# Kernel tuning notes

Hardware: AMD Instinct MI355X
Metric: run time of the kernel (lower is better)

Reference implementation:

```python
import jax, jax.numpy as jnp
import numpy as np

E = 1024  # embedding_dim
A = 1024  # attention_dim


def setup_inputs() -> dict:
    key = jax.random.key(0)
    k0, k1, k2, k3 = jax.random.split(key, 4)
    embedded = jax.random.normal(k0, (4, 4096, E), dtype=jnp.float32)
    # torch Linear weight is [out, in]; stored here as [in, out] for x @ W
    scale = 1.0 / np.sqrt(E)
    Wk = jax.random.uniform(k1, (E, A), dtype=jnp.float32, minval=-scale, maxval=scale)
    Wq = jax.random.uniform(k2, (E, A), dtype=jnp.float32, minval=-scale, maxval=scale)
    Wv = jax.random.uniform(k3, (E, A), dtype=jnp.float32, minval=-scale, maxval=scale)
    return {"embedded": embedded, "Wk": Wk, "Wq": Wq, "Wv": Wv}


def reference(embedded, Wk, Wq, Wv):
    B, T, C = embedded.shape
    K = embedded @ Wk  # [B,T,A]
    Q = embedded @ Wq
    V = embedded @ Wv
    d_k = Q.shape[-1]
    scores = jnp.einsum('bqa,bka->bqk', Q, K) / jnp.sqrt(jnp.float32(d_k))
    causal = jnp.tril(jnp.ones((T, T), dtype=bool))
    scores = jnp.where(causal, scores, -jnp.inf)
    attn = jax.nn.softmax(scores, axis=-1)
    out = jnp.einsum('bqk,bka->bqa', attn, V)
    return jnp.round(out, decimals=4)
```

## Files before the change

### kernel.cpp

```cpp
#include <hip/hip_runtime.h>
#include <hip/hip_fp16.h>

#define T_SEQ 4096
#define NBATCH 4
#define EDIM 1024
#define ADIM 1024
#define MTOT (NBATCH * T_SEQ)

typedef _Float16 f16x8 __attribute__((ext_vector_type(8)));
typedef float f32x4 __attribute__((ext_vector_type(4)));

#define STAGE(SRC, LD, LDSARR)                                               \
  {                                                                          \
    _Pragma("unroll") for (int t = 0; t < 2; ++t) {                          \
      const int rb = w * 2 + t;                                              \
      const _Float16* gsrc =                                                 \
          (SRC) + (size_t)(rb * 16 + (lane & 15)) * (LD) + (lane >> 4) * 8;  \
      __builtin_amdgcn_global_load_lds(                                      \
          (const __attribute__((address_space(1))) void*)gsrc,               \
          (__attribute__((address_space(3))) void*)&LDSARR[rb * 512], 16,    \
          0, 0);                                                             \
    }                                                                        \
  }

#define FRAG(LDSARR, B4, G) (*(const f16x8*)&LDSARR[((B4) * 4 + (G)) * 128 + lr * 8])

__global__ __launch_bounds__(256) void cast_x(const float* __restrict__ X,
                                              _Float16* __restrict__ Xh) {
  const size_t i = ((size_t)blockIdx.x * 256 + threadIdx.x) * 8;
  float4 a = ((const float4*)(X + i))[0];
  float4 b = ((const float4*)(X + i))[1];
  f16x8 o = {(_Float16)a.x, (_Float16)a.y, (_Float16)a.z, (_Float16)a.w,
             (_Float16)b.x, (_Float16)b.y, (_Float16)b.z, (_Float16)b.w};
  *(f16x8*)(Xh + i) = o;
}

__global__ __launch_bounds__(256) void cast_transpose_w(
    const float* __restrict__ Wk, const float* __restrict__ Wq,
    const float* __restrict__ Wv, _Float16* __restrict__ Wt) {
  __shared__ float tile[32][33];
  const int z = blockIdx.z;
  const float* W = (z == 0) ? Wk : (z == 1) ? Wq : Wv;
  const int n0 = blockIdx.x * 32, k0 = blockIdx.y * 32;
  const int tx = threadIdx.x, ty = threadIdx.y;
#pragma unroll
  for (int yy = 0; yy < 32; yy += 8)
    tile[ty + yy][tx] = W[(size_t)(k0 + ty + yy) * ADIM + n0 + tx];
  __syncthreads();
  _Float16* out = Wt + (size_t)z * EDIM * ADIM;
#pragma unroll
  for (int yy = 0; yy < 32; yy += 8)
    out[(size_t)(n0 + ty + yy) * EDIM + k0 + tx] = (_Float16)tile[tx][ty + yy];
}

__global__ __launch_bounds__(256) void gemm_qkv(
    const _Float16* __restrict__ Xh, const _Float16* __restrict__ Wt,
    _Float16* __restrict__ Qb, _Float16* __restrict__ Kb,
    _Float16* __restrict__ Vt) {
  const int z = blockIdx.z;
  const _Float16* Bt = Wt + (size_t)z * EDIM * ADIM;
  __shared__ __align__(16) _Float16 Al[4096];
  __shared__ __align__(16) _Float16 Bl[4096];
  const int tid = threadIdx.x;
  const int lane = tid & 63, w = tid >> 6;
  const int wm = w >> 1, wn = w & 1;
  const int lr = lane & 15, g = lane >> 4;
  const int h = blockIdx.y * gridDim.x + blockIdx.x;
  const int orig = (h & 7) * 128 + (h >> 3);
  const int m0 = (orig >> 3) * 128, n0 = (orig & 7) * 128;

  f32x4 acc[4][4] = {};

  for (int k0 = 0; k0 < EDIM; k0 += 32) {
    STAGE(Xh + (size_t)m0 * EDIM + k0, EDIM, Al);
    STAGE(Bt + (size_t)n0 * EDIM + k0, EDIM, Bl);
    __syncthreads();
    f16x8 af[4], bf[4];
#pragma unroll
    for (int i = 0; i < 4; i++) af[i] = FRAG(Al, wm * 4 + i, g);
#pragma unroll
    for (int j = 0; j < 4; j++) bf[j] = FRAG(Bl, wn * 4 + j, g);
#pragma unroll
    for (int i = 0; i < 4; i++)
#pragma unroll
      for (int j = 0; j < 4; j++)
        acc[i][j] = __builtin_amdgcn_mfma_f32_16x16x32_f16(af[i], bf[j], acc[i][j], 0, 0, 0);
    __syncthreads();
  }

#pragma unroll
  for (int i = 0; i < 4; i++)
#pragma unroll
    for (int j = 0; j < 4; j++)
#pragma unroll
      for (int r = 0; r < 4; r++) {
        const int row = m0 + wm * 64 + i * 16 + 4 * g + r;
        const int col = n0 + wn * 64 + j * 16 + lr;
        const _Float16 hv = (_Float16)acc[i][j][r];
        if (z == 0)
          Kb[(size_t)row * ADIM + col] = hv;
        else if (z == 1)
          Qb[(size_t)row * ADIM + col] = hv;
        else {
          const int b = row >> 12, tt = row & 4095;
          Vt[((size_t)b * ADIM + col) * T_SEQ + tt] = hv;
        }
      }
}

__global__ __launch_bounds__(256) void gemm_sqk(
    const _Float16* __restrict__ Qb, const _Float16* __restrict__ Kb,
    _Float16* __restrict__ Sb) {
  __shared__ __align__(16) _Float16 Al[4096];
  __shared__ __align__(16) _Float16 Bl[4096];
  const int b = blockIdx.y;
  const int tid = threadIdx.x;
  const int lane = tid & 63, w = tid >> 6;
  const int wm = w >> 1, wn = w & 1;
  const int lr = lane & 15, g = lane >> 4;
  const int h = blockIdx.x;
  const int orig = (h & 7) * 66 + (h >> 3);
  int bi = (int)((sqrtf(8.f * orig + 1.f) - 1.f) * 0.5f);
  while ((bi + 1) * (bi + 2) / 2 <= orig) ++bi;
  while (bi * (bi + 1) / 2 > orig) --bi;
  const int bj = orig - bi * (bi + 1) / 2;
  const int m0 = bi * 128, n0 = bj * 128;
  const _Float16* A = Qb + (size_t)b * T_SEQ * ADIM;
  const _Float16* B = Kb + (size_t)b * T_SEQ * ADIM;

  f32x4 acc[4][4] = {};

  for (int k0 = 0; k0 < ADIM; k0 += 32) {
    STAGE(A + (size_t)m0 * ADIM + k0, ADIM, Al);
    STAGE(B + (size_t)n0 * ADIM + k0, ADIM, Bl);
    __syncthreads();
    f16x8 af[4], bf[4];
#pragma unroll
    for (int i = 0; i < 4; i++) af[i] = FRAG(Al, wm * 4 + i, g);
#pragma unroll
    for (int j = 0; j < 4; j++) bf[j] = FRAG(Bl, wn * 4 + j, g);
#pragma unroll
    for (int i = 0; i < 4; i++)
#pragma unroll
      for (int j = 0; j < 4; j++)
        acc[i][j] = __builtin_amdgcn_mfma_f32_16x16x32_f16(af[i], bf[j], acc[i][j], 0, 0, 0);
    __syncthreads();
  }

  _Float16* Srow = Sb + (size_t)b * T_SEQ * T_SEQ;
#pragma unroll
  for (int i = 0; i < 4; i++)
#pragma unroll
    for (int j = 0; j < 4; j++)
#pragma unroll
      for (int r = 0; r < 4; r++) {
        const int row = m0 + wm * 64 + i * 16 + 4 * g + r;
        const int col = n0 + wn * 64 + j * 16 + lr;
        Srow[(size_t)row * T_SEQ + col] = (_Float16)acc[i][j][r];
      }
}

__global__ __launch_bounds__(512) void softmax_rows(_Float16* __restrict__ S) {
  const int i = blockIdx.x, b = blockIdx.y;
  const int padded = ((i >> 7) + 1) << 7;
  const int tid = threadIdx.x;
  const int lane = tid & 63, w = tid >> 6;
  const int j0 = tid * 8;
  const bool active = j0 < padded;
  _Float16* row = S + ((size_t)b * T_SEQ + i) * T_SEQ;
  const float sm_scale = 0.03125f;

  float v[8];
  float m = -1e30f;
  if (active) {
    f16x8 x = *(const f16x8*)(row + j0);
#pragma unroll
    for (int jj = 0; jj < 8; jj++) {
      const float sv = (j0 + jj <= i) ? (float)x[jj] * sm_scale : -1e30f;
      v[jj] = sv;
      m = fmaxf(m, sv);
    }
  } else {
#pragma unroll
    for (int jj = 0; jj < 8; jj++) v[jj] = -1e30f;
  }
#pragma unroll
  for (int off = 1; off < 64; off <<= 1) m = fmaxf(m, __shfl_xor(m, off));
  __shared__ float redm[8], reds[8];
  if (lane == 0) redm[w] = m;
  __syncthreads();
#pragma unroll
  for (int ww = 0; ww < 8; ww++) m = fmaxf(m, redm[ww]);

  float s = 0.f;
#pragma unroll
  for (int jj = 0; jj < 8; jj++) {
    v[jj] = __expf(v[jj] - m);
    s += v[jj];
  }
#pragma unroll
  for (int off = 1; off < 64; off <<= 1) s += __shfl_xor(s, off);
  if (lane == 0) reds[w] = s;
  __syncthreads();
  s = 0.f;
#pragma unroll
  for (int ww = 0; ww < 8; ww++) s += reds[ww];
  const float inv = 1.f / s;

  if (active) {
    f16x8 o;
#pragma unroll
    for (int jj = 0; jj < 8; jj++) o[jj] = (_Float16)(v[jj] * inv);
    *(f16x8*)(row + j0) = o;
  }
}

__global__ __launch_bounds__(256) void gemm_pv(
    const _Float16* __restrict__ Pb, const _Float16* __restrict__ Vt,
    float* __restrict__ Part, float* __restrict__ Out) {
  __shared__ __align__(16) _Float16 Al[4096];
  __shared__ __align__(16) _Float16 Bl[4096];
  const int b = blockIdx.y;
  const int tid = threadIdx.x;
  const int lane = tid & 63, w = tid >> 6;
  const int wm = w >> 1, wn = w & 1;
  const int lr = lane & 15, g = lane >> 4;
  const int h = blockIdx.x;
  const int orig = (h & 7) * 48 + (h >> 3);
  int by, c, bx;
  if (orig < 128) {
    by = orig >> 3; c = 0; bx = orig & 7;
  } else {
    const int idx = orig - 128;
    by = 16 + (idx >> 4); c = (idx >> 3) & 1; bx = idx & 7;
  }
  const int m0 = by * 128, n0 = bx * 128;
  const int kbeg = c * 2048;
  const int kmax = (by + 1) * 128;
  const int kend = (c == 0) ? (kmax < 2048 ? kmax : 2048) : kmax;
  const _Float16* A = Pb + (size_t)b * T_SEQ * T_SEQ;
  const _Float16* B = Vt + (size_t)b * ADIM * T_SEQ;

  f32x4 acc[4][4] = {};

  for (int k0 = kbeg; k0 < kend; k0 += 32) {
    STAGE(A + (size_t)m0 * T_SEQ + k0, T_SEQ, Al);
    STAGE(B + (size_t)n0 * T_SEQ + k0, T_SEQ, Bl);
    __syncthreads();
    f16x8 af[4], bf[4];
#pragma unroll
    for (int i = 0; i < 4; i++) af[i] = FRAG(Al, wm * 4 + i, g);
#pragma unroll
    for (int j = 0; j < 4; j++) bf[j] = FRAG(Bl, wn * 4 + j, g);
#pragma unroll
    for (int i = 0; i < 4; i++)
#pragma unroll
      for (int j = 0; j < 4; j++)
        acc[i][j] = __builtin_amdgcn_mfma_f32_16x16x32_f16(af[i], bf[j], acc[i][j], 0, 0, 0);
    __syncthreads();
  }

#pragma unroll
  for (int i = 0; i < 4; i++)
#pragma unroll
    for (int j = 0; j < 4; j++)
#pragma unroll
      for (int r = 0; r < 4; r++) {
        const int row = m0 + wm * 64 + i * 16 + 4 * g + r;
        const int col = n0 + wn * 64 + j * 16 + lr;
        if (c == 0)
          Out[((size_t)b * T_SEQ + row) * ADIM + col] = acc[i][j][r];
        else
          Part[((size_t)b * 2048 + (row - 2048)) * ADIM + col] = acc[i][j][r];
      }
}

__global__ __launch_bounds__(256) void reduce_pv(const float* __restrict__ Part,
                                                 float* __restrict__ Out) {
  const size_t id = (size_t)blockIdx.x * 256 + threadIdx.x;
  const int b = (int)(id >> 19);
  const size_t rem = id & 524287;
  const size_t row2 = rem >> 8, coli = rem & 255;
  float4* o = (float4*)Out + ((size_t)(b * 4096 + 2048) + row2) * 256 + coli;
  const float4* p = (const float4*)Part + ((size_t)b * 2048 + row2) * 256 + coli;
  float4 ov = *o;
  const float4 pv = *p;
  ov.x += pv.x; ov.y += pv.y; ov.z += pv.z; ov.w += pv.w;
  *o = ov;
}

extern "C" void kernel_launch(void* const* d_in, const int* in_sizes, int n_in,
                              void* d_out, int out_size, void* d_ws, size_t ws_size,
                              hipStream_t stream) {
  const float* X = (const float*)d_in[0];
  const float* Wk = (const float*)d_in[1];
  const float* Wq = (const float*)d_in[2];
  const float* Wv = (const float*)d_in[3];
  float* Out = (float*)d_out;

  char* ws = (char*)d_ws;
  const size_t WT_BYTES = (size_t)3 * EDIM * ADIM * 2;
  const size_t MAT_BYTES = (size_t)MTOT * ADIM * 2;
  _Float16* Wt = (_Float16*)ws;
  _Float16* Kb = (_Float16*)(ws + WT_BYTES);
  _Float16* Qb = (_Float16*)(ws + WT_BYTES + MAT_BYTES);
  _Float16* Vt = (_Float16*)(ws + WT_BYTES + 2 * MAT_BYTES);
  _Float16* Xh = (_Float16*)(ws + WT_BYTES + 3 * MAT_BYTES);
  _Float16* Sb = (_Float16*)(ws + WT_BYTES + 3 * MAT_BYTES);
  float* Part = (float*)Qb;

  cast_x<<<dim3(MTOT * EDIM / 2048), dim3(256), 0, stream>>>(X, Xh);
  cast_transpose_w<<<dim3(32, 32, 3), dim3(32, 8), 0, stream>>>(Wk, Wq, Wv, Wt);
  gemm_qkv<<<dim3(8, 128, 3), dim3(256), 0, stream>>>(Xh, Wt, Qb, Kb, Vt);
  gemm_sqk<<<dim3(528, NBATCH), dim3(256), 0, stream>>>(Qb, Kb, Sb);
  softmax_rows<<<dim3(T_SEQ, NBATCH), dim3(512), 0, stream>>>(Sb);
  gemm_pv<<<dim3(384, NBATCH), dim3(256), 0, stream>>>(Sb, Vt, Part, Out);
  reduce_pv<<<dim3(NBATCH * 2048 * 1024 / 4 / 256), dim3(256), 0, stream>>>(Part, Out);
}
```

Baseline: 695.0 us.

## Double-buffer LDS tiles in the QKV, QK and PV GEMMs to overlap loads

Each of the three MFMA GEMM kernels now uses two LDS buffers per operand. A prologue loads the first K-slice. Each iteration then issues the async global-to-LDS load for the next slice before computing on the current one, leaving one barrier per iteration instead of two. This is meant to hide global load latency behind MFMA work, at the cost of doubling LDS per block, which may lower occupancy.

Result: slower. 715.4 us (+2.9%).

```diff
diff --git a/kernel.cpp b/kernel.cpp
--- a/kernel.cpp
+++ b/kernel.cpp
@@ -18,12 +18,12 @@
           (SRC) + (size_t)(rb * 16 + (lane & 15)) * (LD) + (lane >> 4) * 8;  \
       __builtin_amdgcn_global_load_lds(                                      \
           (const __attribute__((address_space(1))) void*)gsrc,               \
-          (__attribute__((address_space(3))) void*)&LDSARR[rb * 512], 16,    \
+          (__attribute__((address_space(3))) void*)&(LDSARR)[rb * 512], 16,  \
           0, 0);                                                             \
     }                                                                        \
   }
 
-#define FRAG(LDSARR, B4, G) (*(const f16x8*)&LDSARR[((B4) * 4 + (G)) * 128 + lr * 8])
+#define FRAG(LDSARR, B4, G) (*(const f16x8*)&(LDSARR)[((B4) * 4 + (G)) * 128 + lr * 8])
 
 __global__ __launch_bounds__(256) void cast_x(const float* __restrict__ X,
                                               _Float16* __restrict__ Xh) {
@@ -59,8 +59,8 @@
     _Float16* __restrict__ Vt) {
   const int z = blockIdx.z;
   const _Float16* Bt = Wt + (size_t)z * EDIM * ADIM;
-  __shared__ __align__(16) _Float16 Al[4096];
-  __shared__ __align__(16) _Float16 Bl[4096];
+  __shared__ __align__(16) _Float16 Al[2][4096];
+  __shared__ __align__(16) _Float16 Bl[2][4096];
   const int tid = threadIdx.x;
   const int lane = tid & 63, w = tid >> 6;
   const int wm = w >> 1, wn = w & 1;
@@ -68,24 +68,33 @@
   const int h = blockIdx.y * gridDim.x + blockIdx.x;
   const int orig = (h & 7) * 128 + (h >> 3);
   const int m0 = (orig >> 3) * 128, n0 = (orig & 7) * 128;
+  const _Float16* Abase = Xh + (size_t)m0 * EDIM;
+  const _Float16* Bbase = Bt + (size_t)n0 * EDIM;
 
   f32x4 acc[4][4] = {};
 
+  STAGE(Abase, EDIM, Al[0]);
+  STAGE(Bbase, EDIM, Bl[0]);
+  __syncthreads();
+  int cur = 0;
   for (int k0 = 0; k0 < EDIM; k0 += 32) {
-    STAGE(Xh + (size_t)m0 * EDIM + k0, EDIM, Al);
-    STAGE(Bt + (size_t)n0 * EDIM + k0, EDIM, Bl);
-    __syncthreads();
+    const int nxt = cur ^ 1;
+    if (k0 + 32 < EDIM) {
+      STAGE(Abase + k0 + 32, EDIM, Al[nxt]);
+      STAGE(Bbase + k0 + 32, EDIM, Bl[nxt]);
+    }
     f16x8 af[4], bf[4];
 #pragma unroll
-    for (int i = 0; i < 4; i++) af[i] = FRAG(Al, wm * 4 + i, g);
-#pragma unroll
-    for (int j = 0; j < 4; j++) bf[j] = FRAG(Bl, wn * 4 + j, g);
+    for (int i = 0; i < 4; i++) af[i] = FRAG(Al[cur], wm * 4 + i, g);
+#pragma unroll
+    for (int j = 0; j < 4; j++) bf[j] = FRAG(Bl[cur], wn * 4 + j, g);
 #pragma unroll
     for (int i = 0; i < 4; i++)
 #pragma unroll
       for (int j = 0; j < 4; j++)
         acc[i][j] = __builtin_amdgcn_mfma_f32_16x16x32_f16(af[i], bf[j], acc[i][j], 0, 0, 0);
     __syncthreads();
+    cur = nxt;
   }
 
 #pragma unroll
@@ -111,8 +120,8 @@
 __global__ __launch_bounds__(256) void gemm_sqk(
     const _Float16* __restrict__ Qb, const _Float16* __restrict__ Kb,
     _Float16* __restrict__ Sb) {
-  __shared__ __align__(16) _Float16 Al[4096];
-  __shared__ __align__(16) _Float16 Bl[4096];
+  __shared__ __align__(16) _Float16 Al[2][4096];
+  __shared__ __align__(16) _Float16 Bl[2][4096];
   const int b = blockIdx.y;
   const int tid = threadIdx.x;
   const int lane = tid & 63, w = tid >> 6;
@@ -125,26 +134,33 @@
   while (bi * (bi + 1) / 2 > orig) --bi;
   const int bj = orig - bi * (bi + 1) / 2;
   const int m0 = bi * 128, n0 = bj * 128;
-  const _Float16* A = Qb + (size_t)b * T_SEQ * ADIM;
-  const _Float16* B = Kb + (size_t)b * T_SEQ * ADIM;
+  const _Float16* Abase = Qb + (size_t)b * T_SEQ * ADIM + (size_t)m0 * ADIM;
+  const _Float16* Bbase = Kb + (size_t)b * T_SEQ * ADIM + (size_t)n0 * ADIM;
 
   f32x4 acc[4][4] = {};
 
+  STAGE(Abase, ADIM, Al[0]);
+  STAGE(Bbase, ADIM, Bl[0]);
+  __syncthreads();
+  int cur = 0;
   for (int k0 = 0; k0 < ADIM; k0 += 32) {
-    STAGE(A + (size_t)m0 * ADIM + k0, ADIM, Al);
-    STAGE(B + (size_t)n0 * ADIM + k0, ADIM, Bl);
-    __syncthreads();
+    const int nxt = cur ^ 1;
+    if (k0 + 32 < ADIM) {
+      STAGE(Abase + k0 + 32, ADIM, Al[nxt]);
+      STAGE(Bbase + k0 + 32, ADIM, Bl[nxt]);
+    }
     f16x8 af[4], bf[4];
 #pragma unroll
-    for (int i = 0; i < 4; i++) af[i] = FRAG(Al, wm * 4 + i, g);
-#pragma unroll
-    for (int j = 0; j < 4; j++) bf[j] = FRAG(Bl, wn * 4 + j, g);
+    for (int i = 0; i < 4; i++) af[i] = FRAG(Al[cur], wm * 4 + i, g);
+#pragma unroll
+    for (int j = 0; j < 4; j++) bf[j] = FRAG(Bl[cur], wn * 4 + j, g);
 #pragma unroll
     for (int i = 0; i < 4; i++)
 #pragma unroll
       for (int j = 0; j < 4; j++)
         acc[i][j] = __builtin_amdgcn_mfma_f32_16x16x32_f16(af[i], bf[j], acc[i][j], 0, 0, 0);
     __syncthreads();
+    cur = nxt;
   }
 
   _Float16* Srow = Sb + (size_t)b * T_SEQ * T_SEQ;
@@ -218,8 +234,8 @@
 __global__ __launch_bounds__(256) void gemm_pv(
     const _Float16* __restrict__ Pb, const _Float16* __restrict__ Vt,
     float* __restrict__ Part, float* __restrict__ Out) {
-  __shared__ __align__(16) _Float16 Al[4096];
-  __shared__ __align__(16) _Float16 Bl[4096];
+  __shared__ __align__(16) _Float16 Al[2][4096];
+  __shared__ __align__(16) _Float16 Bl[2][4096];
   const int b = blockIdx.y;
   const int tid = threadIdx.x;
   const int lane = tid & 63, w = tid >> 6;
@@ -238,26 +254,33 @@
   const int kbeg = c * 2048;
   const int kmax = (by + 1) * 128;
   const int kend = (c == 0) ? (kmax < 2048 ? kmax : 2048) : kmax;
-  const _Float16* A = Pb + (size_t)b * T_SEQ * T_SEQ;
-  const _Float16* B = Vt + (size_t)b * ADIM * T_SEQ;
+  const _Float16* Abase = Pb + (size_t)b * T_SEQ * T_SEQ + (size_t)m0 * T_SEQ;
+  const _Float16* Bbase = Vt + (size_t)b * ADIM * T_SEQ + (size_t)n0 * T_SEQ;
 
   f32x4 acc[4][4] = {};
 
+  STAGE(Abase + kbeg, T_SEQ, Al[0]);
+  STAGE(Bbase + kbeg, T_SEQ, Bl[0]);
+  __syncthreads();
+  int cur = 0;
   for (int k0 = kbeg; k0 < kend; k0 += 32) {
-    STAGE(A + (size_t)m0 * T_SEQ + k0, T_SEQ, Al);
-    STAGE(B + (size_t)n0 * T_SEQ + k0, T_SEQ, Bl);
-    __syncthreads();
+    const int nxt = cur ^ 1;
+    if (k0 + 32 < kend) {
+      STAGE(Abase + k0 + 32, T_SEQ, Al[nxt]);
+      STAGE(Bbase + k0 + 32, T_SEQ, Bl[nxt]);
+    }
     f16x8 af[4], bf[4];
 #pragma unroll
-    for (int i = 0; i < 4; i++) af[i] = FRAG(Al, wm * 4 + i, g);
-#pragma unroll
-    for (int j = 0; j < 4; j++) bf[j] = FRAG(Bl, wn * 4 + j, g);
+    for (int i = 0; i < 4; i++) af[i] = FRAG(Al[cur], wm * 4 + i, g);
+#pragma unroll
+    for (int j = 0; j < 4; j++) bf[j] = FRAG(Bl[cur], wn * 4 + j, g);
 #pragma unroll
     for (int i = 0; i < 4; i++)
 #pragma unroll
       for (int j = 0; j < 4; j++)
         acc[i][j] = __builtin_amdgcn_mfma_f32_16x16x32_f16(af[i], bf[j], acc[i][j], 0, 0, 0);
     __syncthreads();
+    cur = nxt;
   }
 
 #pragma unroll
```

## Move V transpose to separate kernel and double K-step per sync in GEMMs

Applied to the files above, without the earlier changes.

The QKV GEMM now writes V row-major with coalesced stores. A new LDS-tiled transpose kernel then produces the transposed V layout, replacing the scattered strided 2-byte stores in the GEMM epilogue. All three GEMMs also stage two 32-wide K slices per iteration with doubled LDS, which halves the number of barrier pairs. The cost is an extra kernel launch, an extra pass over V, and more LDS per block, which may lower occupancy.

After: 701.0 us. About the same (+0.9%).

```diff
diff --git a/kernel.cpp b/kernel.cpp
--- a/kernel.cpp
+++ b/kernel.cpp
@@ -18,12 +18,12 @@
           (SRC) + (size_t)(rb * 16 + (lane & 15)) * (LD) + (lane >> 4) * 8;  \
       __builtin_amdgcn_global_load_lds(                                      \
           (const __attribute__((address_space(1))) void*)gsrc,               \
-          (__attribute__((address_space(3))) void*)&LDSARR[rb * 512], 16,    \
+          (__attribute__((address_space(3))) void*)&(LDSARR)[rb * 512], 16,  \
           0, 0);                                                             \
     }                                                                        \
   }
 
-#define FRAG(LDSARR, B4, G) (*(const f16x8*)&LDSARR[((B4) * 4 + (G)) * 128 + lr * 8])
+#define FRAG(LDSARR, B4, G) (*(const f16x8*)&(LDSARR)[((B4) * 4 + (G)) * 128 + lr * 8])
 
 __global__ __launch_bounds__(256) void cast_x(const float* __restrict__ X,
                                               _Float16* __restrict__ Xh) {
@@ -56,11 +56,11 @@
 __global__ __launch_bounds__(256) void gemm_qkv(
     const _Float16* __restrict__ Xh, const _Float16* __restrict__ Wt,
     _Float16* __restrict__ Qb, _Float16* __restrict__ Kb,
-    _Float16* __restrict__ Vt) {
+    _Float16* __restrict__ Vr) {
   const int z = blockIdx.z;
   const _Float16* Bt = Wt + (size_t)z * EDIM * ADIM;
-  __shared__ __align__(16) _Float16 Al[4096];
-  __shared__ __align__(16) _Float16 Bl[4096];
+  __shared__ __align__(16) _Float16 Al[8192];
+  __shared__ __align__(16) _Float16 Bl[8192];
   const int tid = threadIdx.x;
   const int lane = tid & 63, w = tid >> 6;
   const int wm = w >> 1, wn = w & 1;
@@ -68,26 +68,34 @@
   const int h = blockIdx.y * gridDim.x + blockIdx.x;
   const int orig = (h & 7) * 128 + (h >> 3);
   const int m0 = (orig >> 3) * 128, n0 = (orig & 7) * 128;
+  const _Float16* Abase = Xh + (size_t)m0 * EDIM;
+  const _Float16* Bbase = Bt + (size_t)n0 * EDIM;
 
   f32x4 acc[4][4] = {};
 
-  for (int k0 = 0; k0 < EDIM; k0 += 32) {
-    STAGE(Xh + (size_t)m0 * EDIM + k0, EDIM, Al);
-    STAGE(Bt + (size_t)n0 * EDIM + k0, EDIM, Bl);
-    __syncthreads();
-    f16x8 af[4], bf[4];
-#pragma unroll
-    for (int i = 0; i < 4; i++) af[i] = FRAG(Al, wm * 4 + i, g);
-#pragma unroll
-    for (int j = 0; j < 4; j++) bf[j] = FRAG(Bl, wn * 4 + j, g);
-#pragma unroll
-    for (int i = 0; i < 4; i++)
-#pragma unroll
-      for (int j = 0; j < 4; j++)
-        acc[i][j] = __builtin_amdgcn_mfma_f32_16x16x32_f16(af[i], bf[j], acc[i][j], 0, 0, 0);
-    __syncthreads();
-  }
-
+  for (int k0 = 0; k0 < EDIM; k0 += 64) {
+    STAGE(Abase + k0, EDIM, Al);
+    STAGE(Abase + k0 + 32, EDIM, Al + 4096);
+    STAGE(Bbase + k0, EDIM, Bl);
+    STAGE(Bbase + k0 + 32, EDIM, Bl + 4096);
+    __syncthreads();
+#pragma unroll
+    for (int s = 0; s < 2; ++s) {
+      f16x8 af[4], bf[4];
+#pragma unroll
+      for (int i = 0; i < 4; i++) af[i] = FRAG(Al + s * 4096, wm * 4 + i, g);
+#pragma unroll
+      for (int j = 0; j < 4; j++) bf[j] = FRAG(Bl + s * 4096, wn * 4 + j, g);
+#pragma unroll
+      for (int i = 0; i < 4; i++)
+#pragma unroll
+        for (int j = 0; j < 4; j++)
+          acc[i][j] = __builtin_amdgcn_mfma_f32_16x16x32_f16(af[i], bf[j], acc[i][j], 0, 0, 0);
+    }
+    __syncthreads();
+  }
+
+  _Float16* Outz = (z == 0) ? Kb : (z == 1) ? Qb : Vr;
 #pragma unroll
   for (int i = 0; i < 4; i++)
 #pragma unroll
@@ -96,23 +104,42 @@
       for (int r = 0; r < 4; r++) {
         const int row = m0 + wm * 64 + i * 16 + 4 * g + r;
         const int col = n0 + wn * 64 + j * 16 + lr;
-        const _Float16 hv = (_Float16)acc[i][j][r];
-        if (z == 0)
-          Kb[(size_t)row * ADIM + col] = hv;
-        else if (z == 1)
-          Qb[(size_t)row * ADIM + col] = hv;
-        else {
-          const int b = row >> 12, tt = row & 4095;
-          Vt[((size_t)b * ADIM + col) * T_SEQ + tt] = hv;
-        }
+        Outz[(size_t)row * ADIM + col] = (_Float16)acc[i][j][r];
       }
+}
+
+__global__ __launch_bounds__(256) void transpose_v(
+    const _Float16* __restrict__ Vr, _Float16* __restrict__ Vt) {
+  __shared__ _Float16 t[64][72];
+  const int b = blockIdx.z;
+  const int f0 = blockIdx.x * 64, t0 = blockIdx.y * 64;
+  const int tid = threadIdx.x;
+  const int c8 = tid & 7;
+  const int r = tid >> 3;
+  const _Float16* src = Vr + (size_t)b * T_SEQ * ADIM;
+#pragma unroll
+  for (int it = 0; it < 2; ++it) {
+    const int tok = t0 + r + it * 32;
+    *(f16x8*)&t[r + it * 32][c8 * 8] =
+        *(const f16x8*)(src + (size_t)tok * ADIM + f0 + c8 * 8);
+  }
+  __syncthreads();
+  _Float16* dst = Vt + (size_t)b * ADIM * T_SEQ;
+#pragma unroll
+  for (int it = 0; it < 2; ++it) {
+    const int fr = r + it * 32;
+    f16x8 o;
+#pragma unroll
+    for (int j = 0; j < 8; j++) o[j] = t[c8 * 8 + j][fr];
+    *(f16x8*)(dst + (size_t)(f0 + fr) * T_SEQ + t0 + c8 * 8) = o;
+  }
 }
 
 __global__ __launch_bounds__(256) void gemm_sqk(
     const _Float16* __restrict__ Qb, const _Float16* __restrict__ Kb,
     _Float16* __restrict__ Sb) {
-  __shared__ __align__(16) _Float16 Al[4096];
-  __shared__ __align__(16) _Float16 Bl[4096];
+  __shared__ __align__(16) _Float16 Al[8192];
+  __shared__ __align__(16) _Float16 Bl[8192];
   const int b = blockIdx.y;
   const int tid = threadIdx.x;
   const int lane = tid & 63, w = tid >> 6;
@@ -125,25 +152,30 @@
   while (bi * (bi + 1) / 2 > orig) --bi;
   const int bj = orig - bi * (bi + 1) / 2;
   const int m0 = bi * 128, n0 = bj * 128;
-  const _Float16* A = Qb + (size_t)b * T_SEQ * ADIM;
-  const _Float16* B = Kb + (size_t)b * T_SEQ * ADIM;
+  const _Float16* Abase = Qb + (size_t)b * T_SEQ * ADIM + (size_t)m0 * ADIM;
+  const _Float16* Bbase = Kb + (size_t)b * T_SEQ * ADIM + (size_t)n0 * ADIM;
 
   f32x4 acc[4][4] = {};
 
-  for (int k0 = 0; k0 < ADIM; k0 += 32) {
-    STAGE(A + (size_t)m0 * ADIM + k0, ADIM, Al);
-    STAGE(B + (size_t)n0 * ADIM + k0, ADIM, Bl);
-    __syncthreads();
-    f16x8 af[4], bf[4];
-#pragma unroll
-    for (int i = 0; i < 4; i++) af[i] = FRAG(Al, wm * 4 + i, g);
-#pragma unroll
-    for (int j = 0; j < 4; j++) bf[j] = FRAG(Bl, wn * 4 + j, g);
-#pragma unroll
-    for (int i = 0; i < 4; i++)
-#pragma unroll
-      for (int j = 0; j < 4; j++)
-        acc[i][j] = __builtin_amdgcn_mfma_f32_16x16x32_f16(af[i], bf[j], acc[i][j], 0, 0, 0);
+  for (int k0 = 0; k0 < ADIM; k0 += 64) {
+    STAGE(Abase + k0, ADIM, Al);
+    STAGE(Abase + k0 + 32, ADIM, Al + 4096);
+    STAGE(Bbase + k0, ADIM, Bl);
+    STAGE(Bbase + k0 + 32, ADIM, Bl + 4096);
+    __syncthreads();
+#pragma unroll
+    for (int s = 0; s < 2; ++s) {
+      f16x8 af[4], bf[4];
+#pragma unroll
+      for (int i = 0; i < 4; i++) af[i] = FRAG(Al + s * 4096, wm * 4 + i, g);
+#pragma unroll
+      for (int j = 0; j < 4; j++) bf[j] = FRAG(Bl + s * 4096, wn * 4 + j, g);
+#pragma unroll
+      for (int i = 0; i < 4; i++)
+#pragma unroll
+        for (int j = 0; j < 4; j++)
+          acc[i][j] = __builtin_amdgcn_mfma_f32_16x16x32_f16(af[i], bf[j], acc[i][j], 0, 0, 0);
+    }
     __syncthreads();
   }
 
@@ -218,8 +250,8 @@
 __global__ __launch_bounds__(256) void gemm_pv(
     const _Float16* __restrict__ Pb, const _Float16* __restrict__ Vt,
     float* __restrict__ Part, float* __restrict__ Out) {
-  __shared__ __align__(16) _Float16 Al[4096];
-  __shared__ __align__(16) _Float16 Bl[4096];
+  __shared__ __align__(16) _Float16 Al[8192];
+  __shared__ __align__(16) _Float16 Bl[8192];
   const int b = blockIdx.y;
   const int tid = threadIdx.x;
   const int lane = tid & 63, w = tid >> 6;
@@ -238,25 +270,30 @@
   const int kbeg = c * 2048;
   const int kmax = (by + 1) * 128;
   const int kend = (c == 0) ? (kmax < 2048 ? kmax : 2048) : kmax;
-  const _Float16* A = Pb + (size_t)b * T_SEQ * T_SEQ;
-  const _Float16* B = Vt + (size_t)b * ADIM * T_SEQ;
+  const _Float16* Abase = Pb + (size_t)b * T_SEQ * T_SEQ + (size_t)m0 * T_SEQ;
+  const _Float16* Bbase = Vt + (size_t)b * ADIM * T_SEQ + (size_t)n0 * T_SEQ;
 
   f32x4 acc[4][4] = {};
 
-  for (int k0 = kbeg; k0 < kend; k0 += 32) {
-    STAGE(A + (size_t)m0 * T_SEQ + k0, T_SEQ, Al);
-    STAGE(B + (size_t)n0 * T_SEQ + k0, T_SEQ, Bl);
-    __syncthreads();
-    f16x8 af[4], bf[4];
-#pragma unroll
-    for (int i = 0; i < 4; i++) af[i] = FRAG(Al, wm * 4 + i, g);
-#pragma unroll
-    for (int j = 0; j < 4; j++) bf[j] = FRAG(Bl, wn * 4 + j, g);
-#pragma unroll
-    for (int i = 0; i < 4; i++)
-#pragma unroll
-      for (int j = 0; j < 4; j++)
-        acc[i][j] = __builtin_amdgcn_mfma_f32_16x16x32_f16(af[i], bf[j], acc[i][j], 0, 0, 0);
+  for (int k0 = kbeg; k0 < kend; k0 += 64) {
+    STAGE(Abase + k0, T_SEQ, Al);
+    STAGE(Abase + k0 + 32, T_SEQ, Al + 4096);
+    STAGE(Bbase + k0, T_SEQ, Bl);
+    STAGE(Bbase + k0 + 32, T_SEQ, Bl + 4096);
+    __syncthreads();
+#pragma unroll
+    for (int s = 0; s < 2; ++s) {
+      f16x8 af[4], bf[4];
+#pragma unroll
+      for (int i = 0; i < 4; i++) af[i] = FRAG(Al + s * 4096, wm * 4 + i, g);
+#pragma unroll
+      for (int j = 0; j < 4; j++) bf[j] = FRAG(Bl + s * 4096, wn * 4 + j, g);
+#pragma unroll
+      for (int i = 0; i < 4; i++)
+#pragma unroll
+        for (int j = 0; j < 4; j++)
+          acc[i][j] = __builtin_amdgcn_mfma_f32_16x16x32_f16(af[i], bf[j], acc[i][j], 0, 0, 0);
+    }
     __syncthreads();
   }
 
@@ -307,11 +344,13 @@
   _Float16* Vt = (_Float16*)(ws + WT_BYTES + 2 * MAT_BYTES);
   _Float16* Xh = (_Float16*)(ws + WT_BYTES + 3 * MAT_BYTES);
   _Float16* Sb = (_Float16*)(ws + WT_BYTES + 3 * MAT_BYTES);
+  _Float16* Vr = (_Float16*)(ws + WT_BYTES + 4 * MAT_BYTES);
   float* Part = (float*)Qb;
 
   cast_x<<<dim3(MTOT * EDIM / 2048), dim3(256), 0, stream>>>(X, Xh);
   cast_transpose_w<<<dim3(32, 32, 3), dim3(32, 8), 0, stream>>>(Wk, Wq, Wv, Wt);
-  gemm_qkv<<<dim3(8, 128, 3), dim3(256), 0, stream>>>(Xh, Wt, Qb, Kb, Vt);
+  gemm_qkv<<<dim3(8, 128, 3), dim3(256), 0, stream>>>(Xh, Wt, Qb, Kb, Vr);
+  transpose_v<<<dim3(ADIM / 64, T_SEQ / 64, NBATCH), dim3(256), 0, stream>>>(Vr, Vt);
   gemm_sqk<<<dim3(528, NBATCH), dim3(256), 0, stream>>>(Qb, Kb, Sb);
   softmax_rows<<<dim3(T_SEQ, NBATCH), dim3(512), 0, stream>>>(Sb);
   gemm_pv<<<dim3(384, NBATCH), dim3(256), 0, stream>>>(Sb, Vt, Part, Out);
```
